# Kernel optimization log

Measured on AMD Instinct MI355X. Metric: run time of the kernel, lower is better.

## Reference

```python
import jax, jax.numpy as jnp
import numpy as np

HIDDEN = 1024
HEADS = 16
HEAD_DIM = HIDDEN // HEADS


def setup_inputs() -> dict:
    key = jax.random.key(0)
    ks = jax.random.split(key, 8)
    B, S = 2, 2048
    scale = 1.0 / np.sqrt(HIDDEN)
    inp = {
        "hidden_states": jax.random.normal(ks[0], (B, S, HIDDEN), dtype=jnp.float32),
        "attention_mask": jnp.zeros((B, 1, 1, S), dtype=jnp.float32),
        "q_w": jax.random.normal(ks[1], (HIDDEN, HIDDEN), dtype=jnp.float32) * scale,
        "q_b": jnp.zeros((HIDDEN,), dtype=jnp.float32),
        "k_w": jax.random.normal(ks[2], (HIDDEN, HIDDEN), dtype=jnp.float32) * scale,
        "k_b": jnp.zeros((HIDDEN,), dtype=jnp.float32),
        "v_w": jax.random.normal(ks[3], (HIDDEN, HIDDEN), dtype=jnp.float32) * scale,
        "v_b": jnp.zeros((HIDDEN,), dtype=jnp.float32),
    }
    return inp


def _split_heads(x):
    # [B, S, H] -> [B, heads, S, head_dim]
    B, S, _ = x.shape
    return x.reshape(B, S, HEADS, HEAD_DIM).transpose(0, 2, 1, 3)


def reference(hidden_states, attention_mask, q_w, q_b, k_w, k_b, v_w, v_b):
    # Linear projections (torch Linear: x @ W.T + b; here weights stored as [in, out])
    q = _split_heads(hidden_states @ q_w + q_b)  # [B, h, S, d]
    k = _split_heads(hidden_states @ k_w + k_b)
    v = _split_heads(hidden_states @ v_w + v_b)

    scores = jnp.einsum("bhqd,bhkd->bhqk", q, k) / jnp.sqrt(jnp.float32(HEAD_DIM))
    scores = scores + attention_mask  # additive mask, broadcast [B,1,1,S]
    probs = jax.nn.softmax(scores, axis=-1)
    # dropout prob = 0.0 -> identity
    ctx = jnp.einsum("bhqk,bhkd->bhqd", probs, v)  # [B, h, S, d]
    B, _, S, _ = ctx.shape
    ctx = ctx.transpose(0, 2, 1, 3).reshape(B, S, HIDDEN)
    return ctx
```

## Files before the change

### kernel.cpp

```cpp
#include <hip/hip_runtime.h>

typedef __bf16 bf16;
typedef __attribute__((ext_vector_type(8))) __bf16 bf16x8;
typedef __attribute__((ext_vector_type(4))) __bf16 bf16x4;
typedef __attribute__((ext_vector_type(4))) float f32x4;

#define MFMA(a, b, c) __builtin_amdgcn_mfma_f32_16x16x32_bf16((a), (b), (c), 0, 0, 0)
#define LOG2E 1.44269504088896340736f

__device__ __forceinline__ bf16x8 cvt8(float4 a, float4 b) {
  bf16x8 r;
  r[0] = (bf16)a.x; r[1] = (bf16)a.y; r[2] = (bf16)a.z; r[3] = (bf16)a.w;
  r[4] = (bf16)b.x; r[5] = (bf16)b.y; r[6] = (bf16)b.z; r[7] = (bf16)b.w;
  return r;
}

__device__ __forceinline__ void stage16(const bf16* g, bf16* l) {
  __builtin_amdgcn_global_load_lds(
      (const __attribute__((address_space(1))) void*)g,
      (__attribute__((address_space(3))) void*)l, 16, 0, 0);
}

__global__ __launch_bounds__(256)
void cvt(const float* __restrict__ hs, const float* __restrict__ qw,
         const float* __restrict__ kw, const float* __restrict__ vw,
         bf16* __restrict__ Xb, bf16* __restrict__ Wt) {
  const int bid = blockIdx.x, tid = threadIdx.x;
  if (bid < 2048) {
    size_t off = (size_t)bid * 2048 + tid * 8;
    float4 x0 = *(const float4*)(hs + off);
    float4 x1 = *(const float4*)(hs + off + 4);
    *(bf16x8*)(Xb + off) = cvt8(x0, x1);
  } else {
    int t = bid - 2048;
    int z = t >> 8, ti = t & 255;
    const float* W = (z == 0) ? qw : (z == 1) ? kw : vw;
    int k0 = (ti >> 4) * 64, n0 = (ti & 15) * 64;
    __shared__ bf16 T[64 * 72];
    #pragma unroll
    for (int i = 0; i < 16; ++i) {
      int e = i * 256 + tid;
      int kr = e >> 6, nc = e & 63;
      T[nc * 72 + kr] = (bf16)W[(size_t)(k0 + kr) * 1024 + n0 + nc];
    }
    __syncthreads();
    #pragma unroll
    for (int i = 0; i < 2; ++i) {
      int e = i * 256 + tid;
      int nr = e >> 3, kg = e & 7;
      *(bf16x8*)(Wt + (size_t)z * 1048576 + (size_t)(n0 + nr) * 1024 + k0 + kg * 8) =
          *(const bf16x8*)&T[nr * 72 + kg * 8];
    }
  }
}

__global__ __launch_bounds__(256, 3)
void qkv_gemm(const bf16* __restrict__ Xb, const bf16* __restrict__ Wt,
              const float* __restrict__ qbias, const float* __restrict__ kbias,
              const float* __restrict__ vbias,
              bf16* __restrict__ qo, bf16* __restrict__ ko, bf16* __restrict__ vo) {
  const int blk = blockIdx.x;
  const int xcd = blk & 7, slot = blk >> 3;
  const int mb = xcd * 4 + slot / 24;
  const int nb = slot % 24;
  const int z = nb >> 3, nbm = nb & 7;
  const bf16* W = Wt + (size_t)z * 1048576;

  const int tid = threadIdx.x;
  const int wave = tid >> 6, lane = tid & 63, quad = lane >> 4, c = lane & 15;
  const int wr = wave >> 1, wc = wave & 1;
  const int lrow = lane >> 3;
  const int lg = (lane & 7) ^ lrow;

  __shared__ bf16 As[128 * 64];
  __shared__ bf16 Bs[128 * 64];

  f32x4 acc[4][4] = {};

  for (int k0 = 0; k0 < 1024; k0 += 64) {
    #pragma unroll
    for (int i = 0; i < 4; ++i) {
      int r = wave * 32 + i * 8;
      stage16(Xb + (size_t)(mb * 128 + r + lrow) * 1024 + k0 + lg * 8, &As[r * 64]);
      stage16(W + (size_t)(nbm * 128 + r + lrow) * 1024 + k0 + lg * 8, &Bs[r * 64]);
    }
    __syncthreads();
    #pragma unroll
    for (int ch = 0; ch < 2; ++ch) {
      bf16x8 af[4];
      #pragma unroll
      for (int rt = 0; rt < 4; ++rt) {
        int row = wr * 64 + rt * 16 + c;
        af[rt] = *(const bf16x8*)&As[row * 64 + ((((ch << 2) | quad) ^ (c & 7)) << 3)];
      }
      #pragma unroll
      for (int nt = 0; nt < 4; ++nt) {
        int row = wc * 64 + nt * 16 + c;
        bf16x8 bfrag = *(const bf16x8*)&Bs[row * 64 + ((((ch << 2) | quad) ^ (c & 7)) << 3)];
        #pragma unroll
        for (int rt = 0; rt < 4; ++rt)
          acc[rt][nt] = MFMA(af[rt], bfrag, acc[rt][nt]);
      }
    }
    __syncthreads();
  }

  const float* bias = (z == 0) ? qbias : (z == 1) ? kbias : vbias;
  float bv[4];
  #pragma unroll
  for (int nt = 0; nt < 4; ++nt)
    bv[nt] = bias[nbm * 128 + wc * 64 + nt * 16 + c];

  if (z == 2) {
    #pragma unroll
    for (int rt = 0; rt < 4; ++rt)
      #pragma unroll
      for (int nt = 0; nt < 4; ++nt) {
        int m0 = mb * 128 + wr * 64 + rt * 16 + 4 * quad;
        int n = nbm * 128 + wc * 64 + nt * 16 + c;
        bf16x4 pk;
        #pragma unroll
        for (int reg = 0; reg < 4; ++reg) pk[reg] = (bf16)(acc[rt][nt][reg] + bv[nt]);
        int b = m0 >> 11, s0 = m0 & 2047, h = n >> 6, d = n & 63;
        *(bf16x4*)&vo[(((size_t)b * 16 + h) * 64 + d) * 2048 + s0] = pk;
      }
  } else {
    bf16* dst = (z == 0) ? qo : ko;
    const float scale = (z == 0) ? 0.125f * LOG2E : 1.0f;
    #pragma unroll
    for (int rt = 0; rt < 4; ++rt)
      #pragma unroll
      for (int nt = 0; nt < 4; ++nt)
        #pragma unroll
        for (int reg = 0; reg < 4; ++reg) {
          float v = (acc[rt][nt][reg] + bv[nt]) * scale;
          int m = mb * 128 + wr * 64 + rt * 16 + 4 * quad + reg;
          int n = nbm * 128 + wc * 64 + nt * 16 + c;
          int b = m >> 11, s = m & 2047, h = n >> 6, d = n & 63;
          dst[(((size_t)b * 16 + h) * 2048 + s) * 64 + d] = (bf16)v;
        }
  }
}

__global__ __launch_bounds__(256, 2)
void attn(const bf16* __restrict__ qg, const bf16* __restrict__ kg,
          const bf16* __restrict__ vtg, const float* __restrict__ mask,
          float* __restrict__ out) {
  const int blk = blockIdx.x;
  const int xcd = blk & 7, slot = blk >> 3;
  const int bh = xcd * 4 + (slot >> 4);
  const int qblk = slot & 15;
  const int b = bh >> 4, h = bh & 15;
  const int tid = threadIdx.x;
  const int wave = tid >> 6, lane = tid & 63, quad = lane >> 4, c = lane & 15;
  const int lrow = lane >> 3, lg = (lane & 7) ^ lrow;

  __shared__ __align__(16) bf16 Ks[2][64 * 64];
  __shared__ __align__(16) bf16 Vs[2][64 * 64];
  __shared__ __align__(16) bf16 Ps[4][2][16 * 68];

  const bf16* qb_ = qg + (size_t)bh * 2048 * 64;
  const bf16* kb_ = kg + (size_t)bh * 2048 * 64;
  const bf16* vb_ = vtg + (size_t)bh * 64 * 2048;

  bf16x8 qf[2][2];
  #pragma unroll
  for (int ct = 0; ct < 2; ++ct)
    #pragma unroll
    for (int ch = 0; ch < 2; ++ch)
      qf[ct][ch] = *(const bf16x8*)(qb_ +
          (size_t)(qblk * 128 + wave * 32 + ct * 16 + c) * 64 + ch * 32 + quad * 8);

  f32x4 o[2][4] = {};
  float lsum[2] = {0.f, 0.f};

  #pragma unroll
  for (int i = 0; i < 2; ++i) {
    int r = wave * 16 + i * 8;
    stage16(kb_ + (size_t)(r + lrow) * 64 + lg * 8, &Ks[0][r * 64]);
    stage16(vb_ + (size_t)(r + lrow) * 2048 + lg * 8, &Vs[0][r * 64]);
  }
  __asm__ volatile("s_waitcnt vmcnt(0)" ::: "memory");
  __builtin_amdgcn_s_barrier();

  for (int kt = 0; kt < 32; ++kt) {
    const int cur = kt & 1;

    if (kt < 31) {
      #pragma unroll
      for (int i = 0; i < 2; ++i) {
        int r = wave * 16 + i * 8;
        stage16(kb_ + (size_t)((kt + 1) * 64 + r + lrow) * 64 + lg * 8,
                &Ks[cur ^ 1][r * 64]);
        stage16(vb_ + (size_t)(r + lrow) * 2048 + (kt + 1) * 64 + lg * 8,
                &Vs[cur ^ 1][r * 64]);
      }
    }
    __builtin_amdgcn_sched_barrier(0);

    float4 mv[4];
    #pragma unroll
    for (int nt = 0; nt < 4; ++nt)
      mv[nt] = *(const float4*)&mask[b * 2048 + kt * 64 + nt * 16 + 4 * quad];

    f32x4 s[2][4] = {};
    #pragma unroll
    for (int nt = 0; nt < 4; ++nt)
      #pragma unroll
      for (int ch = 0; ch < 2; ++ch) {
        bf16x8 kf = *(const bf16x8*)&Ks[cur][(nt * 16 + c) * 64 +
                                            ((((ch << 2) | quad) ^ (c & 7)) << 3)];
        #pragma unroll
        for (int ct = 0; ct < 2; ++ct)
          s[ct][nt] = MFMA(kf, qf[ct][ch], s[ct][nt]);
      }

    #pragma unroll
    for (int ct = 0; ct < 2; ++ct)
      #pragma unroll
      for (int nt = 0; nt < 4; ++nt) {
        bf16x4 pk;
        #pragma unroll
        for (int reg = 0; reg < 4; ++reg) {
          float mreg = (reg == 0) ? mv[nt].x : (reg == 1) ? mv[nt].y
                     : (reg == 2) ? mv[nt].z : mv[nt].w;
          float p = __builtin_amdgcn_exp2f(s[ct][nt][reg] + mreg * LOG2E);
          lsum[ct] += p;
          pk[reg] = (bf16)p;
        }
        int g = (nt * 2 + (quad >> 1)) ^ (c & 7);
        *(bf16x4*)&Ps[wave][ct][c * 68 + g * 8 + (quad & 1) * 4] = pk;
      }
    __asm__ volatile("s_waitcnt lgkmcnt(0)" ::: "memory");

    #pragma unroll
    for (int ch = 0; ch < 2; ++ch) {
      bf16x8 pa[2];
      #pragma unroll
      for (int ct = 0; ct < 2; ++ct) {
        int gp = ((ch << 2) | quad) ^ (c & 7);
        bf16x4 lo = *(const bf16x4*)&Ps[wave][ct][c * 68 + gp * 8];
        bf16x4 hi = *(const bf16x4*)&Ps[wave][ct][c * 68 + gp * 8 + 4];
        pa[ct][0] = lo[0]; pa[ct][1] = lo[1]; pa[ct][2] = lo[2]; pa[ct][3] = lo[3];
        pa[ct][4] = hi[0]; pa[ct][5] = hi[1]; pa[ct][6] = hi[2]; pa[ct][7] = hi[3];
      }
      #pragma unroll
      for (int nt = 0; nt < 4; ++nt) {
        bf16x8 vf = *(const bf16x8*)&Vs[cur][(nt * 16 + c) * 64 +
                                            ((((ch << 2) | quad) ^ (c & 7)) << 3)];
        #pragma unroll
        for (int ct = 0; ct < 2; ++ct)
          o[ct][nt] = MFMA(vf, pa[ct], o[ct][nt]);
      }
    }

    __asm__ volatile("s_waitcnt vmcnt(0) lgkmcnt(0)" ::: "memory");
    __builtin_amdgcn_s_barrier();
  }

  #pragma unroll
  for (int ct = 0; ct < 2; ++ct) {
    float l = lsum[ct];
    l += __shfl_xor(l, 16, 64);
    l += __shfl_xor(l, 32, 64);
    const float inv = 1.0f / l;
    const int srow = qblk * 128 + wave * 32 + ct * 16 + c;
    #pragma unroll
    for (int nt = 0; nt < 4; ++nt) {
      float4 st = { o[ct][nt][0] * inv, o[ct][nt][1] * inv,
                    o[ct][nt][2] * inv, o[ct][nt][3] * inv };
      *(float4*)&out[((size_t)b * 2048 + srow) * 1024 + h * 64 + nt * 16 + 4 * quad] = st;
    }
  }
}

extern "C" void kernel_launch(void* const* d_in, const int* in_sizes, int n_in,
                              void* d_out, int out_size, void* d_ws, size_t ws_size,
                              hipStream_t stream) {
  const float* hs   = (const float*)d_in[0];
  const float* mask = (const float*)d_in[1];
  const float* qw   = (const float*)d_in[2];
  const float* qb   = (const float*)d_in[3];
  const float* kw   = (const float*)d_in[4];
  const float* kb   = (const float*)d_in[5];
  const float* vw   = (const float*)d_in[6];
  const float* vb   = (const float*)d_in[7];
  float* out = (float*)d_out;

  bf16* Xb   = (bf16*)d_ws;
  bf16* Wt   = Xb + (size_t)4096 * 1024;
  bf16* q_ws = Wt + (size_t)3 * 1048576;
  bf16* k_ws = q_ws + (size_t)4096 * 1024;
  bf16* v_ws = k_ws + (size_t)4096 * 1024;

  cvt<<<dim3(2816), 256, 0, stream>>>(hs, qw, kw, vw, Xb, Wt);
  qkv_gemm<<<dim3(768), 256, 0, stream>>>(Xb, Wt, qb, kb, vb, q_ws, k_ws, v_ws);
  attn<<<dim3(512), 256, 0, stream>>>(q_ws, k_ws, v_ws, mask, out);
}
```

Baseline: 176.9 us.

## Triple-buffer K/V, permlane P transpose, LDS-cached scaled mask, MFMA priority

Adds a third K/V buffer and prefetches two tiles ahead, waiting with a partial vmcnt so loads stay in flight across iterations. The P matrix now reaches MFMA operand layout through v_permlane32/16_swap in registers instead of an LDS round-trip. The mask is preloaded into LDS already multiplied by log2e, which removes per-tile global mask reads and one multiply per element. s_setprio is raised around the MFMA blocks. The trade-off is more LDS for K/V and the mask, which may limit occupancy, plus finer synchronisation that is easier to get wrong.

```diff
diff --git a/kernel.cpp b/kernel.cpp
--- a/kernel.cpp
+++ b/kernel.cpp
@@ -4,6 +4,8 @@
 typedef __attribute__((ext_vector_type(8))) __bf16 bf16x8;
 typedef __attribute__((ext_vector_type(4))) __bf16 bf16x4;
 typedef __attribute__((ext_vector_type(4))) float f32x4;
+typedef __attribute__((ext_vector_type(2))) unsigned int uint2v;
+typedef __attribute__((ext_vector_type(4))) unsigned int uint4v;
 
 #define MFMA(a, b, c) __builtin_amdgcn_mfma_f32_16x16x32_bf16((a), (b), (c), 0, 0, 0)
 #define LOG2E 1.44269504088896340736f
@@ -155,14 +157,22 @@
   const int wave = tid >> 6, lane = tid & 63, quad = lane >> 4, c = lane & 15;
   const int lrow = lane >> 3, lg = (lane & 7) ^ lrow;
 
-  __shared__ __align__(16) bf16 Ks[2][64 * 64];
-  __shared__ __align__(16) bf16 Vs[2][64 * 64];
-  __shared__ __align__(16) bf16 Ps[4][2][16 * 68];
+  __shared__ __align__(16) bf16 Ks[3][64 * 64];
+  __shared__ __align__(16) bf16 Vs[3][64 * 64];
+  __shared__ __align__(16) float Ms[2048];
 
   const bf16* qb_ = qg + (size_t)bh * 2048 * 64;
   const bf16* kb_ = kg + (size_t)bh * 2048 * 64;
   const bf16* vb_ = vtg + (size_t)bh * 64 * 2048;
 
+  #pragma unroll
+  for (int i = 0; i < 2; ++i) {
+    int idx = i * 1024 + tid * 4;
+    float4 m = *(const float4*)&mask[b * 2048 + idx];
+    float4 ms = {m.x * LOG2E, m.y * LOG2E, m.z * LOG2E, m.w * LOG2E};
+    *(float4*)&Ms[idx] = ms;
+  }
+
   bf16x8 qf[2][2];
   #pragma unroll
   for (int ct = 0; ct < 2; ++ct)
@@ -171,52 +181,63 @@
       qf[ct][ch] = *(const bf16x8*)(qb_ +
           (size_t)(qblk * 128 + wave * 32 + ct * 16 + c) * 64 + ch * 32 + quad * 8);
 
+  #pragma unroll
+  for (int t = 0; t < 2; ++t) {
+    #pragma unroll
+    for (int i = 0; i < 2; ++i) {
+      int r = wave * 16 + i * 8;
+      stage16(kb_ + (size_t)(t * 64 + r + lrow) * 64 + lg * 8, &Ks[t][r * 64]);
+      stage16(vb_ + (size_t)(r + lrow) * 2048 + t * 64 + lg * 8, &Vs[t][r * 64]);
+    }
+    __builtin_amdgcn_sched_barrier(0);
+  }
+  __asm__ volatile("s_waitcnt lgkmcnt(0)" ::: "memory");
+
   f32x4 o[2][4] = {};
   float lsum[2] = {0.f, 0.f};
 
-  #pragma unroll
-  for (int i = 0; i < 2; ++i) {
-    int r = wave * 16 + i * 8;
-    stage16(kb_ + (size_t)(r + lrow) * 64 + lg * 8, &Ks[0][r * 64]);
-    stage16(vb_ + (size_t)(r + lrow) * 2048 + lg * 8, &Vs[0][r * 64]);
-  }
-  __asm__ volatile("s_waitcnt vmcnt(0)" ::: "memory");
-  __builtin_amdgcn_s_barrier();
-
+  int cur = 0;
   for (int kt = 0; kt < 32; ++kt) {
-    const int cur = kt & 1;
-
-    if (kt < 31) {
+    if (kt < 31) { __asm__ volatile("s_waitcnt vmcnt(4)" ::: "memory"); }
+    else         { __asm__ volatile("s_waitcnt vmcnt(0)" ::: "memory"); }
+    __builtin_amdgcn_s_barrier();
+    __builtin_amdgcn_sched_barrier(0);
+
+    if (kt < 30) {
+      int stg = cur - 1; if (stg < 0) stg = 2;
       #pragma unroll
       for (int i = 0; i < 2; ++i) {
         int r = wave * 16 + i * 8;
-        stage16(kb_ + (size_t)((kt + 1) * 64 + r + lrow) * 64 + lg * 8,
-                &Ks[cur ^ 1][r * 64]);
-        stage16(vb_ + (size_t)(r + lrow) * 2048 + (kt + 1) * 64 + lg * 8,
-                &Vs[cur ^ 1][r * 64]);
+        stage16(kb_ + (size_t)((kt + 2) * 64 + r + lrow) * 64 + lg * 8,
+                &Ks[stg][r * 64]);
+        stage16(vb_ + (size_t)(r + lrow) * 2048 + (kt + 2) * 64 + lg * 8,
+                &Vs[stg][r * 64]);
       }
     }
     __builtin_amdgcn_sched_barrier(0);
 
-    float4 mv[4];
-    #pragma unroll
-    for (int nt = 0; nt < 4; ++nt)
-      mv[nt] = *(const float4*)&mask[b * 2048 + kt * 64 + nt * 16 + 4 * quad];
-
     f32x4 s[2][4] = {};
+    __builtin_amdgcn_s_setprio(1);
     #pragma unroll
     for (int nt = 0; nt < 4; ++nt)
       #pragma unroll
       for (int ch = 0; ch < 2; ++ch) {
         bf16x8 kf = *(const bf16x8*)&Ks[cur][(nt * 16 + c) * 64 +
                                             ((((ch << 2) | quad) ^ (c & 7)) << 3)];
-        #pragma unroll
-        for (int ct = 0; ct < 2; ++ct)
-          s[ct][nt] = MFMA(kf, qf[ct][ch], s[ct][nt]);
-      }
-
-    #pragma unroll
-    for (int ct = 0; ct < 2; ++ct)
+        s[0][nt] = MFMA(kf, qf[0][ch], s[0][nt]);
+        s[1][nt] = MFMA(kf, qf[1][ch], s[1][nt]);
+      }
+    __builtin_amdgcn_s_setprio(0);
+
+    float4 mv[4];
+    #pragma unroll
+    for (int nt = 0; nt < 4; ++nt)
+      mv[nt] = *(const float4*)&Ms[kt * 64 + nt * 16 + 4 * quad];
+
+    bf16x8 pa[2][2];
+    #pragma unroll
+    for (int ct = 0; ct < 2; ++ct) {
+      unsigned int U[4][2];
       #pragma unroll
       for (int nt = 0; nt < 4; ++nt) {
         bf16x4 pk;
@@ -224,38 +245,39 @@
         for (int reg = 0; reg < 4; ++reg) {
           float mreg = (reg == 0) ? mv[nt].x : (reg == 1) ? mv[nt].y
                      : (reg == 2) ? mv[nt].z : mv[nt].w;
-          float p = __builtin_amdgcn_exp2f(s[ct][nt][reg] + mreg * LOG2E);
+          float p = __builtin_amdgcn_exp2f(s[ct][nt][reg] + mreg);
           lsum[ct] += p;
           pk[reg] = (bf16)p;
         }
-        int g = (nt * 2 + (quad >> 1)) ^ (c & 7);
-        *(bf16x4*)&Ps[wave][ct][c * 68 + g * 8 + (quad & 1) * 4] = pk;
-      }
-    __asm__ volatile("s_waitcnt lgkmcnt(0)" ::: "memory");
-
-    #pragma unroll
-    for (int ch = 0; ch < 2; ++ch) {
-      bf16x8 pa[2];
-      #pragma unroll
-      for (int ct = 0; ct < 2; ++ct) {
-        int gp = ((ch << 2) | quad) ^ (c & 7);
-        bf16x4 lo = *(const bf16x4*)&Ps[wave][ct][c * 68 + gp * 8];
-        bf16x4 hi = *(const bf16x4*)&Ps[wave][ct][c * 68 + gp * 8 + 4];
-        pa[ct][0] = lo[0]; pa[ct][1] = lo[1]; pa[ct][2] = lo[2]; pa[ct][3] = lo[3];
-        pa[ct][4] = hi[0]; pa[ct][5] = hi[1]; pa[ct][6] = hi[2]; pa[ct][7] = hi[3];
-      }
+        uint2v uu = __builtin_bit_cast(uint2v, pk);
+        U[nt][0] = uu.x; U[nt][1] = uu.y;
+      }
+      #pragma unroll
+      for (int ch = 0; ch < 2; ++ch) {
+        unsigned int X0 = U[2 * ch][0],     X1 = U[2 * ch][1];
+        unsigned int Y0 = U[2 * ch + 1][0], Y1 = U[2 * ch + 1][1];
+        __asm__ volatile("v_permlane32_swap_b32 %0, %1" : "+v"(X0), "+v"(Y0));
+        __asm__ volatile("v_permlane32_swap_b32 %0, %1" : "+v"(X1), "+v"(Y1));
+        __asm__ volatile("v_permlane16_swap_b32 %0, %1" : "+v"(X0), "+v"(Y0));
+        __asm__ volatile("v_permlane16_swap_b32 %0, %1" : "+v"(X1), "+v"(Y1));
+        uint4v up = {X0, X1, Y0, Y1};
+        pa[ct][ch] = __builtin_bit_cast(bf16x8, up);
+      }
+    }
+
+    __builtin_amdgcn_s_setprio(1);
+    #pragma unroll
+    for (int ch = 0; ch < 2; ++ch)
       #pragma unroll
       for (int nt = 0; nt < 4; ++nt) {
         bf16x8 vf = *(const bf16x8*)&Vs[cur][(nt * 16 + c) * 64 +
                                             ((((ch << 2) | quad) ^ (c & 7)) << 3)];
-        #pragma unroll
-        for (int ct = 0; ct < 2; ++ct)
-          o[ct][nt] = MFMA(vf, pa[ct], o[ct][nt]);
-      }
-    }
-
-    __asm__ volatile("s_waitcnt vmcnt(0) lgkmcnt(0)" ::: "memory");
-    __builtin_amdgcn_s_barrier();
+        o[0][nt] = MFMA(vf, pa[0][ch], o[0][nt]);
+        o[1][nt] = MFMA(vf, pa[1][ch], o[1][nt]);
+      }
+    __builtin_amdgcn_s_setprio(0);
+
+    cur = (cur == 2) ? 0 : cur + 1;
   }
 
   #pragma unroll
```

Result: faster. 163.8 us (-7.4%).
